# Optimization experiments

Hardware: AMD Instinct MI355X
Metric: run time of the kernel (lower is better)

The kernel has to match this reference:

```python
import jax, jax.numpy as jnp
import numpy as np


def setup_inputs() -> dict:
    key = jax.random.key(0)
    k1, k2 = jax.random.split(key)
    B, N, M = 8, 4096, 4096
    xyz1 = jax.random.normal(k1, (B, N, 3), dtype=jnp.float32)
    xyz2 = jax.random.normal(k2, (B, M, 3), dtype=jnp.float32)
    return {"xyz1": xyz1, "xyz2": xyz2}


def _chamfer_sq_dists(xyz1, xyz2):
    # Squared euclidean all-pairs distances via ||a||^2 + ||b||^2 - 2 a.b
    # xyz1: [B,N,3], xyz2: [B,M,3]
    n1 = jnp.sum(xyz1 * xyz1, axis=-1)              # [B,N]
    n2 = jnp.sum(xyz2 * xyz2, axis=-1)              # [B,M]
    dots = jnp.einsum('bnd,bmd->bnm', xyz1, xyz2)   # [B,N,M]
    d2 = n1[:, :, None] + n2[:, None, :] - 2.0 * dots
    dist1 = jnp.min(d2, axis=2)                     # [B,N] min over xyz2
    dist2 = jnp.min(d2, axis=1)                     # [B,M] min over xyz1
    return dist1, dist2


def reference(xyz1, xyz2):
    dist1, dist2 = _chamfer_sq_dists(xyz1, xyz2)
    return jnp.mean(dist1) + jnp.mean(dist2)
```

## Files before the change

### kernel.cpp

```cpp
#include <hip/hip_runtime.h>

typedef float f32x16 __attribute__((ext_vector_type(16)));
typedef short bf16x8 __attribute__((ext_vector_type(8)));

#define BLOCK 256
#define NPTS 4096
#define CHUNK_PTS 256
#define NCHUNK (NPTS / CHUNK_PTS)
#define SUBS (CHUNK_PTS / 32)
#define TW 2
#define TILES_PER_BLOCK 8

__device__ inline unsigned int f2bf(float x) {
    unsigned int u = __float_as_uint(x);
    return (u + 0x7FFFu + ((u >> 16) & 1)) >> 16;
}
__device__ inline float bf2f(unsigned int b) { return __uint_as_float(b << 16); }
__device__ inline unsigned int pk2(unsigned int lo, unsigned int hi) {
    return (hi << 16) | (lo & 0xFFFFu);
}

__global__ __launch_bounds__(BLOCK) void pack_pts(
    const float* __restrict__ x1, const float* __restrict__ x2,
    uint4* __restrict__ arrA, uint4* __restrict__ arrB,
    float* __restrict__ wn, int n1, int ntot, float* __restrict__ out) {
    int i = blockIdx.x * BLOCK + threadIdx.x;
    if (i == 0) out[0] = 0.0f;
    if (i >= ntot) return;
    const float* s = (i < n1) ? x1 + 3 * (size_t)i : x2 + 3 * (size_t)(i - n1);
    float x = s[0], y = s[1], z = s[2];
    float w = fmaf(z, z, fmaf(y, y, x * x));
    wn[i] = w;
    unsigned int hx = f2bf(x), hy = f2bf(y), hz = f2bf(z);
    unsigned int lx = f2bf(x - bf2f(hx)), ly = f2bf(y - bf2f(hy)), lz = f2bf(z - bf2f(hz));
    unsigned int hw = f2bf(w), lw = f2bf(w - bf2f(hw));
    unsigned int ax = f2bf(-2.f * bf2f(hx)), ay = f2bf(-2.f * bf2f(hy)), az = f2bf(-2.f * bf2f(hz));
    unsigned int bx = f2bf(-2.f * bf2f(lx)), by = f2bf(-2.f * bf2f(ly)), bz = f2bf(-2.f * bf2f(lz));
    const unsigned int one = 0x3F80u;
    uint4 A0 = make_uint4(pk2(ax, ay), pk2(az, bx), pk2(by, bz), pk2(ax, ay));
    uint4 A1 = make_uint4(pk2(az, one), pk2(one, 0u), 0u, 0u);
    arrA[(size_t)i * 2 + 0] = A0;
    arrA[(size_t)i * 2 + 1] = A1;
    uint4 B0 = make_uint4(pk2(hx, hy), pk2(hz, hx), pk2(hy, hz), pk2(lx, ly));
    uint4 B1 = make_uint4(pk2(lz, hw), pk2(lw, 0u), 0u, 0u);
    arrB[(size_t)i * 2 + 0] = B0;
    arrB[(size_t)i * 2 + 1] = B1;
}

__global__ __launch_bounds__(BLOCK) void chamfer_mfma(
    const uint4* __restrict__ arrA, const uint4* __restrict__ arrB,
    const float* __restrict__ wn, int n1, int Bc,
    float inv1, float inv2, float* __restrict__ out) {
    __shared__ uint4 lds[CHUNK_PTS * 2];
    __shared__ float red[4];
    int tid = threadIdx.x;
    int lane = tid & 63, widx = tid >> 6;
    int l31 = lane & 31, blk = lane >> 5;

    int bid = blockIdx.x;
    int bd = bid >> 4;
    int seg = bid & 15;
    int dir = (bd >= Bc) ? 1 : 0;
    int b = dir ? bd - Bc : bd;
    int ownOff = dir ? n1 : 0;
    int othOff = dir ? 0 : n1;
    float inv = dir ? inv2 : inv1;

    int tile0 = seg * TILES_PER_BLOCK + widx * TW;
    int row0 = tile0 * 32;

    size_t aBase = (size_t)(ownOff + b * NPTS + row0 + l31) * 2 + blk;
    bf16x8 afA = *(const bf16x8*)(arrA + aBase);
    bf16x8 afB = *(const bf16x8*)(arrA + aBase + 64);

    const uint4* gB = arrB + (size_t)(othOff + b * NPTS) * 2;

    f32x16 runA, runB;
#pragma unroll
    for (int r = 0; r < 16; ++r) { runA[r] = 3.0e38f; runB[r] = 3.0e38f; }

    uint4 p0 = gB[tid], p1 = gB[tid + 256];
    lds[tid] = p0;
    lds[tid + 256] = p1;
    __syncthreads();

    f32x16 zero = {};
    for (int c = 0; c < NCHUNK; ++c) {
        if (c + 1 < NCHUNK) {
            p0 = gB[(c + 1) * 512 + tid];
            p1 = gB[(c + 1) * 512 + 256 + tid];
        }
        const bf16x8* lp = (const bf16x8*)lds;
#pragma unroll
        for (int s = 0; s < SUBS; s += 2) {
            bf16x8 bf0 = lp[(s * 32 + l31) * 2 + blk];
            bf16x8 bf1 = lp[((s + 1) * 32 + l31) * 2 + blk];
            f32x16 acc0a = __builtin_amdgcn_mfma_f32_32x32x16_bf16(afA, bf0, zero, 0, 0, 0);
            f32x16 acc0b = __builtin_amdgcn_mfma_f32_32x32x16_bf16(afB, bf0, zero, 0, 0, 0);
            f32x16 acc1a = __builtin_amdgcn_mfma_f32_32x32x16_bf16(afA, bf1, zero, 0, 0, 0);
            f32x16 acc1b = __builtin_amdgcn_mfma_f32_32x32x16_bf16(afB, bf1, zero, 0, 0, 0);
#pragma unroll
            for (int r = 0; r < 16; ++r) {
                runA[r] = fminf(runA[r], fminf(acc0a[r], acc1a[r]));
                runB[r] = fminf(runB[r], fminf(acc0b[r], acc1b[r]));
            }
        }
        __syncthreads();
        if (c + 1 < NCHUNK) {
            lds[tid] = p0;
            lds[tid + 256] = p1;
        }
        __syncthreads();
    }

#pragma unroll
    for (int m = 1; m <= 16; m <<= 1) {
#pragma unroll
        for (int r = 0; r < 16; ++r) {
            runA[r] = fminf(runA[r], __shfl_xor(runA[r], m, 64));
            runB[r] = fminf(runB[r], __shfl_xor(runB[r], m, 64));
        }
    }
    float contrib = 0.0f;
    if (l31 == 0) {
        const float* wp = wn + ownOff + b * NPTS;
#pragma unroll
        for (int r = 0; r < 16; ++r) {
            int rowA = row0 + ((r & 3) + 8 * (r >> 2) + 4 * blk);
            contrib += runA[r] + wp[rowA];
            contrib += runB[r] + wp[rowA + 32];
        }
    }
    contrib += __shfl_xor(contrib, 32, 64);
    if (lane == 0) red[widx] = contrib * inv;
    __syncthreads();
    if (tid == 0) atomicAdd(out, red[0] + red[1] + red[2] + red[3]);
}

__global__ __launch_bounds__(BLOCK) void chamfer_direct(
    const float* __restrict__ x1, const float* __restrict__ x2,
    int Npts, int Mpts, float inv1, float inv2, float* __restrict__ out) {
    int dir = blockIdx.z;
    const float* own = dir ? x2 : x1;
    const float* oth = dir ? x1 : x2;
    int np = dir ? Mpts : Npts;
    int mp = dir ? Npts : Mpts;
    float scale = dir ? inv2 : inv1;

    int bpb = np / BLOCK;
    int b = blockIdx.x / bpb;
    int i = (blockIdx.x % bpb) * BLOCK + threadIdx.x;

    const float* pp = own + ((size_t)b * np + i) * 3;
    float px = pp[0], py = pp[1], pz = pp[2];
    const float* o = oth + (size_t)b * mp * 3;

    float best = 3.0e38f;
#pragma unroll 4
    for (int j = 0; j < mp; ++j) {
        float dx = px - o[3 * j + 0];
        float dy = py - o[3 * j + 1];
        float dz = pz - o[3 * j + 2];
        float d2 = fmaf(dz, dz, fmaf(dy, dy, dx * dx));
        best = fminf(best, d2);
    }
    float s = best * scale;
    for (int off = 32; off; off >>= 1) s += __shfl_down(s, off, 64);
    __shared__ float red[BLOCK / 64];
    int lane = threadIdx.x & 63, wid = threadIdx.x >> 6;
    if (!lane) red[wid] = s;
    __syncthreads();
    if (!threadIdx.x) atomicAdd(out, red[0] + red[1] + red[2] + red[3]);
}

extern "C" void kernel_launch(void* const* d_in, const int* in_sizes, int n_in,
                              void* d_out, int out_size, void* d_ws, size_t ws_size,
                              hipStream_t stream) {
    const float* xyz1 = (const float*)d_in[0];
    const float* xyz2 = (const float*)d_in[1];
    float* out = (float*)d_out;

    const int Bc = in_sizes[0] / (3 * NPTS);
    const int n1 = Bc * NPTS;
    const int n2 = Bc * NPTS;
    const int ntot = n1 + n2;

    size_t need = (size_t)ntot * (32 + 32 + 4);
    bool okShape = Bc >= 1 && in_sizes[0] == Bc * 3 * NPTS && in_sizes[1] == in_sizes[0];

    if (okShape && ws_size >= need) {
        uint4* arrA = (uint4*)d_ws;
        uint4* arrB = (uint4*)((char*)d_ws + (size_t)ntot * 32);
        float* wn = (float*)((char*)d_ws + (size_t)ntot * 64);

        pack_pts<<<(ntot + BLOCK - 1) / BLOCK, BLOCK, 0, stream>>>(
            xyz1, xyz2, arrA, arrB, wn, n1, ntot, out);

        chamfer_mfma<<<Bc * 2 * 16, BLOCK, 0, stream>>>(
            arrA, arrB, wn, n1, Bc,
            1.0f / (float)n1, 1.0f / (float)n2, out);
    } else {
        hipMemsetAsync(d_out, 0, sizeof(float), stream);
        dim3 grid((in_sizes[0] / 3 / NPTS) * (NPTS / BLOCK), 1, 2);
        chamfer_direct<<<grid, BLOCK, 0, stream>>>(xyz1, xyz2, NPTS, NPTS,
                                                   1.0f / (float)n1, 1.0f / (float)n2, out);
    }
}
```

Baseline: 46.51 us.

## Split scan dimension across blocks with atomicMin merge and double-buffered LDS

Work is repartitioned. Each block now handles 128 rows with one tile per wave and scans only half of the other cloud, so the grid grows from 256 to 1024 blocks. Partial row minima are merged through atomicMin on order-preserving float keys in a workspace array, and a third kernel converts them back and computes the means. The LDS staging is double-buffered, with a de-interleaved layout, so each chunk needs one barrier instead of two. The aim is more occupancy and parallelism across CUs, at the cost of global atomics, an extra launch and a second pass over the data.

```diff
diff --git a/kernel.cpp b/kernel.cpp
--- a/kernel.cpp
+++ b/kernel.cpp
@@ -5,11 +5,12 @@
 
 #define BLOCK 256
 #define NPTS 4096
-#define CHUNK_PTS 256
-#define NCHUNK (NPTS / CHUNK_PTS)
-#define SUBS (CHUNK_PTS / 32)
-#define TW 2
-#define TILES_PER_BLOCK 8
+#define SEGS 32
+#define SCANSPLIT 2
+#define SCANPTS (NPTS / SCANSPLIT)
+#define CHUNK 256
+#define NCHUNK (SCANPTS / CHUNK)
+#define SUBS (CHUNK / 32)
 
 __device__ inline unsigned int f2bf(float x) {
     unsigned int u = __float_as_uint(x);
@@ -19,11 +20,20 @@
 __device__ inline unsigned int pk2(unsigned int lo, unsigned int hi) {
     return (hi << 16) | (lo & 0xFFFFu);
 }
+__device__ inline unsigned int fkey(float f) {
+    unsigned int u = __float_as_uint(f);
+    return (u & 0x80000000u) ? ~u : (u | 0x80000000u);
+}
+__device__ inline float funkey(unsigned int k) {
+    unsigned int u = (k & 0x80000000u) ? (k & 0x7FFFFFFFu) : ~k;
+    return __uint_as_float(u);
+}
 
 __global__ __launch_bounds__(BLOCK) void pack_pts(
     const float* __restrict__ x1, const float* __restrict__ x2,
     uint4* __restrict__ arrA, uint4* __restrict__ arrB,
-    float* __restrict__ wn, int n1, int ntot, float* __restrict__ out) {
+    float* __restrict__ wn, unsigned int* __restrict__ mins,
+    int n1, int ntot, float* __restrict__ out) {
     int i = blockIdx.x * BLOCK + threadIdx.x;
     if (i == 0) out[0] = 0.0f;
     if (i >= ntot) return;
@@ -31,110 +41,108 @@
     float x = s[0], y = s[1], z = s[2];
     float w = fmaf(z, z, fmaf(y, y, x * x));
     wn[i] = w;
+    mins[i] = 0xFFFFFFFFu;
     unsigned int hx = f2bf(x), hy = f2bf(y), hz = f2bf(z);
     unsigned int lx = f2bf(x - bf2f(hx)), ly = f2bf(y - bf2f(hy)), lz = f2bf(z - bf2f(hz));
     unsigned int hw = f2bf(w), lw = f2bf(w - bf2f(hw));
     unsigned int ax = f2bf(-2.f * bf2f(hx)), ay = f2bf(-2.f * bf2f(hy)), az = f2bf(-2.f * bf2f(hz));
     unsigned int bx = f2bf(-2.f * bf2f(lx)), by = f2bf(-2.f * bf2f(ly)), bz = f2bf(-2.f * bf2f(lz));
     const unsigned int one = 0x3F80u;
-    uint4 A0 = make_uint4(pk2(ax, ay), pk2(az, bx), pk2(by, bz), pk2(ax, ay));
-    uint4 A1 = make_uint4(pk2(az, one), pk2(one, 0u), 0u, 0u);
-    arrA[(size_t)i * 2 + 0] = A0;
-    arrA[(size_t)i * 2 + 1] = A1;
-    uint4 B0 = make_uint4(pk2(hx, hy), pk2(hz, hx), pk2(hy, hz), pk2(lx, ly));
-    uint4 B1 = make_uint4(pk2(lz, hw), pk2(lw, 0u), 0u, 0u);
-    arrB[(size_t)i * 2 + 0] = B0;
-    arrB[(size_t)i * 2 + 1] = B1;
+    arrA[(size_t)i * 2 + 0] = make_uint4(pk2(ax, ay), pk2(az, bx), pk2(by, bz), pk2(ax, ay));
+    arrA[(size_t)i * 2 + 1] = make_uint4(pk2(az, one), pk2(one, 0u), 0u, 0u);
+    arrB[(size_t)i * 2 + 0] = make_uint4(pk2(hx, hy), pk2(hz, hx), pk2(hy, hz), pk2(lx, ly));
+    arrB[(size_t)i * 2 + 1] = make_uint4(pk2(lz, hw), pk2(lw, 0u), 0u, 0u);
 }
 
 __global__ __launch_bounds__(BLOCK) void chamfer_mfma(
     const uint4* __restrict__ arrA, const uint4* __restrict__ arrB,
-    const float* __restrict__ wn, int n1, int Bc,
-    float inv1, float inv2, float* __restrict__ out) {
-    __shared__ uint4 lds[CHUNK_PTS * 2];
-    __shared__ float red[4];
+    unsigned int* __restrict__ mins, int n1, int Bc) {
+    __shared__ uint4 lds[2][2][CHUNK];
     int tid = threadIdx.x;
     int lane = tid & 63, widx = tid >> 6;
     int l31 = lane & 31, blk = lane >> 5;
 
     int bid = blockIdx.x;
-    int bd = bid >> 4;
-    int seg = bid & 15;
+    int sh = bid % SCANSPLIT;
+    int t1 = bid / SCANSPLIT;
+    int seg = t1 % SEGS;
+    int bd = t1 / SEGS;
     int dir = (bd >= Bc) ? 1 : 0;
     int b = dir ? bd - Bc : bd;
     int ownOff = dir ? n1 : 0;
     int othOff = dir ? 0 : n1;
-    float inv = dir ? inv2 : inv1;
-
-    int tile0 = seg * TILES_PER_BLOCK + widx * TW;
-    int row0 = tile0 * 32;
+
+    int row0 = seg * 128 + widx * 32;
 
     size_t aBase = (size_t)(ownOff + b * NPTS + row0 + l31) * 2 + blk;
     bf16x8 afA = *(const bf16x8*)(arrA + aBase);
-    bf16x8 afB = *(const bf16x8*)(arrA + aBase + 64);
-
-    const uint4* gB = arrB + (size_t)(othOff + b * NPTS) * 2;
-
-    f32x16 runA, runB;
-#pragma unroll
-    for (int r = 0; r < 16; ++r) { runA[r] = 3.0e38f; runB[r] = 3.0e38f; }
-
-    uint4 p0 = gB[tid], p1 = gB[tid + 256];
-    lds[tid] = p0;
-    lds[tid + 256] = p1;
+
+    const uint4* gB = arrB + (size_t)(othOff + b * NPTS + sh * SCANPTS) * 2;
+
+    f32x16 run;
+#pragma unroll
+    for (int r = 0; r < 16; ++r) run[r] = 3.0e38f;
+
+    uint4 u0 = gB[tid], u1 = gB[tid + 256];
+    lds[0][tid & 1][tid >> 1] = u0;
+    lds[0][tid & 1][128 + (tid >> 1)] = u1;
     __syncthreads();
 
     f32x16 zero = {};
     for (int c = 0; c < NCHUNK; ++c) {
+        int cur = c & 1;
         if (c + 1 < NCHUNK) {
-            p0 = gB[(c + 1) * 512 + tid];
-            p1 = gB[(c + 1) * 512 + 256 + tid];
-        }
-        const bf16x8* lp = (const bf16x8*)lds;
+            u0 = gB[(c + 1) * 512 + tid];
+            u1 = gB[(c + 1) * 512 + 256 + tid];
+        }
+        const uint4* lp = lds[cur][blk];
 #pragma unroll
         for (int s = 0; s < SUBS; s += 2) {
-            bf16x8 bf0 = lp[(s * 32 + l31) * 2 + blk];
-            bf16x8 bf1 = lp[((s + 1) * 32 + l31) * 2 + blk];
-            f32x16 acc0a = __builtin_amdgcn_mfma_f32_32x32x16_bf16(afA, bf0, zero, 0, 0, 0);
-            f32x16 acc0b = __builtin_amdgcn_mfma_f32_32x32x16_bf16(afB, bf0, zero, 0, 0, 0);
-            f32x16 acc1a = __builtin_amdgcn_mfma_f32_32x32x16_bf16(afA, bf1, zero, 0, 0, 0);
-            f32x16 acc1b = __builtin_amdgcn_mfma_f32_32x32x16_bf16(afB, bf1, zero, 0, 0, 0);
-#pragma unroll
-            for (int r = 0; r < 16; ++r) {
-                runA[r] = fminf(runA[r], fminf(acc0a[r], acc1a[r]));
-                runB[r] = fminf(runB[r], fminf(acc0b[r], acc1b[r]));
-            }
+            bf16x8 bf0 = *(const bf16x8*)(lp + s * 32 + l31);
+            bf16x8 bf1 = *(const bf16x8*)(lp + (s + 1) * 32 + l31);
+            f32x16 acc0 = __builtin_amdgcn_mfma_f32_32x32x16_bf16(afA, bf0, zero, 0, 0, 0);
+            f32x16 acc1 = __builtin_amdgcn_mfma_f32_32x32x16_bf16(afA, bf1, zero, 0, 0, 0);
+#pragma unroll
+            for (int r = 0; r < 16; ++r)
+                run[r] = fminf(run[r], fminf(acc0[r], acc1[r]));
+        }
+        if (c + 1 < NCHUNK) {
+            lds[cur ^ 1][tid & 1][tid >> 1] = u0;
+            lds[cur ^ 1][tid & 1][128 + (tid >> 1)] = u1;
         }
         __syncthreads();
-        if (c + 1 < NCHUNK) {
-            lds[tid] = p0;
-            lds[tid + 256] = p1;
-        }
-        __syncthreads();
-    }
-
-#pragma unroll
-    for (int m = 1; m <= 16; m <<= 1) {
+    }
+
+#pragma unroll
+    for (int m = 1; m <= 16; m <<= 1)
+#pragma unroll
+        for (int r = 0; r < 16; ++r)
+            run[r] = fminf(run[r], __shfl_xor(run[r], m, 64));
+
+    if (l31 == 0) {
+        unsigned int* mo = mins + ownOff + b * NPTS;
 #pragma unroll
         for (int r = 0; r < 16; ++r) {
-            runA[r] = fminf(runA[r], __shfl_xor(runA[r], m, 64));
-            runB[r] = fminf(runB[r], __shfl_xor(runB[r], m, 64));
-        }
-    }
-    float contrib = 0.0f;
-    if (l31 == 0) {
-        const float* wp = wn + ownOff + b * NPTS;
-#pragma unroll
-        for (int r = 0; r < 16; ++r) {
-            int rowA = row0 + ((r & 3) + 8 * (r >> 2) + 4 * blk);
-            contrib += runA[r] + wp[rowA];
-            contrib += runB[r] + wp[rowA + 32];
-        }
-    }
-    contrib += __shfl_xor(contrib, 32, 64);
-    if (lane == 0) red[widx] = contrib * inv;
+            int row = row0 + ((r & 3) + 8 * (r >> 2) + 4 * blk);
+            atomicMin(mo + row, fkey(run[r]));
+        }
+    }
+}
+
+__global__ __launch_bounds__(BLOCK) void reduce_means(
+    const unsigned int* __restrict__ mins, const float* __restrict__ wn,
+    int n1, int ntot, float inv1, float inv2, float* __restrict__ out) {
+    float s = 0.0f;
+    for (int i = blockIdx.x * BLOCK + threadIdx.x; i < ntot; i += gridDim.x * BLOCK) {
+        float v = funkey(mins[i]) + wn[i];
+        s += v * (i < n1 ? inv1 : inv2);
+    }
+    for (int off = 32; off; off >>= 1) s += __shfl_down(s, off, 64);
+    __shared__ float red[BLOCK / 64];
+    int lane = threadIdx.x & 63, wid = threadIdx.x >> 6;
+    if (!lane) red[wid] = s;
     __syncthreads();
-    if (tid == 0) atomicAdd(out, red[0] + red[1] + red[2] + red[3]);
+    if (!threadIdx.x) atomicAdd(out, red[0] + red[1] + red[2] + red[3]);
 }
 
 __global__ __launch_bounds__(BLOCK) void chamfer_direct(
@@ -185,20 +193,23 @@
     const int n2 = Bc * NPTS;
     const int ntot = n1 + n2;
 
-    size_t need = (size_t)ntot * (32 + 32 + 4);
+    size_t need = (size_t)ntot * (32 + 32 + 4 + 4);
     bool okShape = Bc >= 1 && in_sizes[0] == Bc * 3 * NPTS && in_sizes[1] == in_sizes[0];
 
     if (okShape && ws_size >= need) {
         uint4* arrA = (uint4*)d_ws;
         uint4* arrB = (uint4*)((char*)d_ws + (size_t)ntot * 32);
         float* wn = (float*)((char*)d_ws + (size_t)ntot * 64);
+        unsigned int* mins = (unsigned int*)((char*)d_ws + (size_t)ntot * 68);
 
         pack_pts<<<(ntot + BLOCK - 1) / BLOCK, BLOCK, 0, stream>>>(
-            xyz1, xyz2, arrA, arrB, wn, n1, ntot, out);
-
-        chamfer_mfma<<<Bc * 2 * 16, BLOCK, 0, stream>>>(
-            arrA, arrB, wn, n1, Bc,
-            1.0f / (float)n1, 1.0f / (float)n2, out);
+            xyz1, xyz2, arrA, arrB, wn, mins, n1, ntot, out);
+
+        chamfer_mfma<<<Bc * 2 * SEGS * SCANSPLIT, BLOCK, 0, stream>>>(
+            arrA, arrB, mins, n1, Bc);
+
+        reduce_means<<<64, BLOCK, 0, stream>>>(mins, wn, n1, ntot,
+                                               1.0f / (float)n1, 1.0f / (float)n2, out);
     } else {
         hipMemsetAsync(d_out, 0, sizeof(float), stream);
         dim3 grid((in_sizes[0] / 3 / NPTS) * (NPTS / BLOCK), 1, 2);
```

After: 39.48 us. 1.18x faster.
